# Kernel optimization log

Hardware: AMD Instinct MI355X
Metric: run time of the kernel (lower is better)

## Reference

```python
import jax, jax.numpy as jnp
import numpy as np

N, E, F_IN, H, G, C = 50000, 800000, 128, 4, 32, 4
NEG_SLOPE = 0.2
EPS_GN = 1e-5


def setup_inputs() -> dict:
    key = jax.random.key(0)
    ks = iter(jax.random.split(key, 64))
    def gl(shape, fan):
        return jax.random.normal(next(ks), shape, jnp.float32) / np.float32(np.sqrt(fan))
    inp = {}
    inp['x'] = jax.random.normal(next(ks), (N, F_IN), jnp.float32)
    inp['edge_index'] = jax.random.randint(next(ks), (2, E), 0, N, dtype=jnp.int32)
    inp['batch'] = jnp.sort(jax.random.randint(next(ks), (N,), 0, G, dtype=jnp.int32))
    inp['Wl1'] = gl((F_IN, H * 64), F_IN); inp['bl1'] = jnp.zeros((H * 64,), jnp.float32)
    inp['Wr1'] = gl((F_IN, H * 64), F_IN); inp['br1'] = jnp.zeros((H * 64,), jnp.float32)
    inp['att1'] = gl((H, 64), 64); inp['bias1'] = jnp.zeros((H * 64,), jnp.float32)
    inp['gw1'] = jnp.ones((H * 64,), jnp.float32); inp['gb1'] = jnp.zeros((H * 64,), jnp.float32); inp['ga1'] = jnp.ones((H * 64,), jnp.float32)
    inp['Wl2'] = gl((256, H * 32), 256); inp['bl2'] = jnp.zeros((H * 32,), jnp.float32)
    inp['Wr2'] = gl((256, H * 32), 256); inp['br2'] = jnp.zeros((H * 32,), jnp.float32)
    inp['att2'] = gl((H, 32), 32); inp['bias2'] = jnp.zeros((H * 32,), jnp.float32)
    inp['gw2'] = jnp.ones((H * 32,), jnp.float32); inp['gb2'] = jnp.zeros((H * 32,), jnp.float32); inp['ga2'] = jnp.ones((H * 32,), jnp.float32)
    # GATv2 layer 3: 128 -> 16, 4 heads averaged (concat=False)
    inp['Wl3'] = gl((128, H * 16), 128); inp['bl3'] = jnp.zeros((H * 16,), jnp.float32)
    inp['Wr3'] = gl((128, H * 16), 128); inp['br3'] = jnp.zeros((H * 16,), jnp.float32)
    inp['att3'] = gl((H, 16), 16); inp['bias3'] = jnp.zeros((16,), jnp.float32)
    inp['gw3'] = jnp.ones((16,), jnp.float32); inp['gb3'] = jnp.zeros((16,), jnp.float32); inp['ga3'] = jnp.ones((16,), jnp.float32)
    # final linear 16 -> C
    inp['linW'] = gl((16, C), 16); inp['linB'] = jnp.zeros((C,), jnp.float32)
    return inp


def _gatv2(x, src, dst, Wl, bl, Wr, br, att, bias, D, concat):
    n = x.shape[0]
    xl = (x @ Wl + bl).reshape(n, H, D)   # source-side transform
    xr = (x @ Wr + br).reshape(n, H, D)   # target-side transform
    m = xl[src] + xr[dst]                  # [E', H, D]
    s = jnp.einsum('ehd,hd->eh', jax.nn.leaky_relu(m, NEG_SLOPE), att)
    smax = jax.ops.segment_max(s, dst, num_segments=n)
    e = jnp.exp(s - smax[dst])
    denom = jax.ops.segment_sum(e, dst, num_segments=n)
    alpha = e / (denom[dst] + 1e-16)       # softmax over incoming edges
    out = jax.ops.segment_sum(alpha[:, :, None] * xl[src], dst, num_segments=n)
    out = out.reshape(n, H * D) if concat else out.mean(axis=1)
    return out + bias


def _graphnorm(x, batch, w, b, a):
    cnt = jnp.maximum(jax.ops.segment_sum(jnp.ones((x.shape[0],), x.dtype), batch, num_segments=G), 1.0)
    mean = jax.ops.segment_sum(x, batch, num_segments=G) / cnt[:, None]
    xc = x - a * mean[batch]
    var = jax.ops.segment_sum(xc * xc, batch, num_segments=G) / cnt[:, None]
    return w * xc / jnp.sqrt(var[batch] + EPS_GN) + b


def reference(x, edge_index, batch,
              Wl1, bl1, Wr1, br1, att1, bias1, gw1, gb1, ga1,
              Wl2, bl2, Wr2, br2, att2, bias2, gw2, gb2, ga2,
              Wl3, bl3, Wr3, br3, att3, bias3, gw3, gb3, ga3,
              linW, linB):
    n = x.shape[0]
    ar = jnp.arange(n, dtype=edge_index.dtype)
    src = jnp.concatenate([edge_index[0], ar])  # add self-loops (PyG default)
    dst = jnp.concatenate([edge_index[1], ar])
    h = jax.nn.relu(_graphnorm(_gatv2(x, src, dst, Wl1, bl1, Wr1, br1, att1, bias1, 64, True), batch, gw1, gb1, ga1))
    h = jax.nn.relu(_graphnorm(_gatv2(h, src, dst, Wl2, bl2, Wr2, br2, att2, bias2, 32, True), batch, gw2, gb2, ga2))
    h = jax.nn.relu(_graphnorm(_gatv2(h, src, dst, Wl3, bl3, Wr3, br3, att3, bias3, 16, False), batch, gw3, gb3, ga3))
    cnt = jnp.maximum(jax.ops.segment_sum(jnp.ones((n,), h.dtype), batch, num_segments=G), 1.0)
    features = jax.ops.segment_sum(h, batch, num_segments=G) / cnt[:, None]  # global mean pool [G,16]
    logits = features @ linW + linB
    return (logits, features)
```

## Files before the change

kernel.cpp:

```cpp
#include <hip/hip_runtime.h>
#include <cstdint>


#define NEG_SLOPE 0.2f

typedef __attribute__((ext_vector_type(8))) short short8;
typedef __attribute__((ext_vector_type(4))) float f32x4;
typedef _Float16 h2 __attribute__((ext_vector_type(2)));
union U16 { uint4 u; short8 s; };

__device__ inline unsigned short f2bf_rne(float x) {
  unsigned u = __float_as_uint(x);
  return (unsigned short)((u + 0x7fff + ((u >> 16) & 1)) >> 16);
}
__device__ inline unsigned short f2h_bits(float x) {
  _Float16 h = (_Float16)x;
  return __builtin_bit_cast(unsigned short, h);
}
__device__ inline float h2f(unsigned short h) {
  return (float)__builtin_bit_cast(_Float16, h);
}
__device__ inline h2 u2h2(unsigned u) { return __builtin_bit_cast(h2, u); }

__device__ inline float fdot2h(h2 a, h2 b, float c) {
#if __has_builtin(__builtin_amdgcn_fdot2)
  return __builtin_amdgcn_fdot2(a, b, c, false);
#else
  return c + (float)a.x * (float)b.x + (float)a.y * (float)b.y;
#endif
}

__device__ inline int wave_incl_scan(int v, int lane) {
#pragma unroll
  for (int ofs = 1; ofs < 64; ofs <<= 1) {
    int t = __shfl_up(v, ofs, 64);
    if (lane >= ofs) v += t;
  }
  return v;
}

__global__ void deg_batch_hist(const int* __restrict__ ei, const int* __restrict__ batch,
                               int* __restrict__ deg, int* __restrict__ cnt, int E, int N) {
  __shared__ int h[32];
  if (threadIdx.x < 32) h[threadIdx.x] = 0;
  __syncthreads();
  int i = blockIdx.x * blockDim.x + threadIdx.x;
  int ET = E + N;
  if (i < ET) {
    int d = (i < E) ? ei[E + i] : (i - E);
    atomicAdd(&deg[d], 1);
  }
  if (i < N) atomicAdd(&h[batch[i]], 1);
  __syncthreads();
  if (threadIdx.x < 32 && h[threadIdx.x] > 0) atomicAdd(&cnt[threadIdx.x], h[threadIdx.x]);
}

__global__ void chunk_sums(const int* __restrict__ deg, int* __restrict__ bsum, int n) {
  int tid = threadIdx.x, lane = tid & 63, wid = tid >> 6;
  int i = blockIdx.x * 1024 + tid;
  int v = (i < n) ? deg[i] : 0;
#pragma unroll
  for (int m = 32; m; m >>= 1) v += __shfl_xor(v, m, 64);
  __shared__ int ws[16];
  if (lane == 0) ws[wid] = v;
  __syncthreads();
  if (tid == 0) {
    int s = 0;
    for (int k = 0; k < 16; ++k) s += ws[k];
    bsum[blockIdx.x] = s;
  }
}

__global__ void scan_apply(const int* __restrict__ deg, const int* __restrict__ bsum,
                           int* __restrict__ off, int nb, int n) {
  __shared__ int ws[16];
  __shared__ int sb[64];
  int tid = threadIdx.x, lane = tid & 63, wid = tid >> 6;
  if (wid == 0) {
    int v = (lane < nb) ? bsum[lane] : 0;
    int incl = wave_incl_scan(v, lane);
    sb[lane] = incl;
  }
  __syncthreads();
  int boff = (blockIdx.x > 0) ? sb[blockIdx.x - 1] : 0;
  if (blockIdx.x == 0 && tid == 0) off[n] = sb[nb - 1];
  int i = blockIdx.x * 1024 + tid;
  int v = (i < n) ? deg[i] : 0;
  int incl = wave_incl_scan(v, lane);
  if (lane == 63) ws[wid] = incl;
  __syncthreads();
  if (wid == 0) {
    int t = (lane < 16) ? ws[lane] : 0;
    t = wave_incl_scan(t, lane);
    if (lane < 16) ws[lane] = t;
  }
  __syncthreads();
  int wpre = (wid > 0) ? ws[wid - 1] : 0;
  if (i < n) off[i] = boff + wpre + incl - v;
}

__global__ void scatter_edges(const int* __restrict__ ei, const int* __restrict__ off,
                              int* __restrict__ cur, int* __restrict__ csr_src,
                              int E, int N) {
  int i = blockIdx.x * blockDim.x + threadIdx.x;
  int ET = E + N;
  if (i >= ET) return;
  int s, d;
  if (i < E) { s = ei[i]; d = ei[E + i]; } else { s = d = i - E; }
  int pos = off[d] + atomicAdd(&cur[d], 1);
  csr_src[pos] = s;
}

__device__ inline void wprep_body(const float* __restrict__ W, unsigned short* __restrict__ pk,
                                  int K, int M, int t) {
  int nk = K >> 5;
  int total = (M >> 4) * nk * 512;
  if (t >= total) return;
  int j = t & 7;
  int l = (t >> 3) & 63;
  int rest = t >> 9;
  int kc = rest % nk;
  int ct = rest / nk;
  int k = (kc << 5) + ((l >> 4) << 3) + j;
  int col = (ct << 4) + (l & 15);
  float w = W[(size_t)k * M + col];
  unsigned u = __float_as_uint(w);
  unsigned short hi = (unsigned short)(u >> 16);
  float hif = __uint_as_float(u & 0xffff0000u);
  unsigned short lo = f2bf_rne(w - hif);
  unsigned short* dst = pk + ((size_t)(ct * nk + kc) * 64 + l) * 16;
  dst[j] = hi;
  dst[j + 8] = lo;
}

__global__ void wprep_all(const float* W0, const float* W1, const float* W2,
                          const float* W3, const float* W4, const float* W5,
                          unsigned short* p0, unsigned short* p1, unsigned short* p2,
                          unsigned short* p3, unsigned short* p4, unsigned short* p5) {
  int t = blockIdx.x * 256 + threadIdx.x;
  switch (blockIdx.y) {
    case 0: wprep_body(W0, p0, 128, 256, t); break;
    case 1: wprep_body(W1, p1, 128, 256, t); break;
    case 2: wprep_body(W2, p2, 256, 128, t); break;
    case 3: wprep_body(W3, p3, 256, 128, t); break;
    case 4: wprep_body(W4, p4, 128, 64, t); break;
    default: wprep_body(W5, p5, 128, 64, t); break;
  }
}

__device__ inline void gemm_epilogue(
    unsigned short* __restrict__ sb0, unsigned short* __restrict__ sb1,
    f32x4* accL, f32x4* accR,
    const float* __restrict__ biasL, const float* __restrict__ biasR,
    unsigned short* __restrict__ CL, unsigned short* __restrict__ CR,
    int N, int M, int c0g, int row0blk) {
  int wv = threadIdx.x >> 6, lane = threadIdx.x & 63;
  int lrow0 = wv * 16 + ((lane >> 4) << 2);
  int lcolb = lane & 15;
#pragma unroll
  for (int ct = 0; ct < 4; ++ct) {
    int lcol = (ct << 4) + lcolb;
    float bvL = biasL[(c0g << 4) + lcol];
    float bvR = biasR[(c0g << 4) + lcol];
#pragma unroll
    for (int r = 0; r < 4; ++r) {
      sb0[(lrow0 + r) * 72 + lcol] = f2h_bits(accL[ct][r] + bvL);
      sb1[(lrow0 + r) * 72 + lcol] = f2h_bits(accR[ct][r] + bvR);
    }
  }
  __syncthreads();
  int tid = threadIdx.x;
#pragma unroll
  for (int pass = 0; pass < 2; ++pass) {
    int row = (tid >> 3) + (pass << 5);
    int gr = row0blk + row;
    if (gr < N) {
      int co = (tid & 7) << 3;
      uint4 vL = *(const uint4*)&sb0[row * 72 + co];
      uint4 vR = *(const uint4*)&sb1[row * 72 + co];
      size_t go = (size_t)gr * M + (c0g << 4) + co;
      *(uint4*)(CL + go) = vL;
      *(uint4*)(CR + go) = vR;
    }
  }
}

__global__ __launch_bounds__(256) void gemm_f32a_dual(
    const float* __restrict__ A,
    const uint4* __restrict__ WpkL, const uint4* __restrict__ WpkR,
    const float* __restrict__ biasL, const float* __restrict__ biasR,
    unsigned short* __restrict__ CL, unsigned short* __restrict__ CR,
    int N, int K, int M) {
  __shared__ unsigned short sb[2][64 * 72];
  int wv = threadIdx.x >> 6, lane = threadIdx.x & 63;
  int r0 = blockIdx.y * 64 + wv * 16;
  int c0g = blockIdx.x << 2;
  int row = r0 + (lane & 15);
  int kq = (lane >> 4) << 3;
  int nk = K >> 5;
  bool rok = row < N;
  const float* arow = A + (size_t)row * K;
  f32x4 accL[4], accR[4];
#pragma unroll
  for (int i = 0; i < 4; ++i) { accL[i] = (f32x4){0,0,0,0}; accR[i] = (f32x4){0,0,0,0}; }
  for (int kc = 0; kc < nk; ++kc) {
    float av[8];
    if (rok) {
      float4 t0 = *(const float4*)(arow + (kc << 5) + kq);
      float4 t1 = *(const float4*)(arow + (kc << 5) + kq + 4);
      av[0] = t0.x; av[1] = t0.y; av[2] = t0.z; av[3] = t0.w;
      av[4] = t1.x; av[5] = t1.y; av[6] = t1.z; av[7] = t1.w;
    } else {
#pragma unroll
      for (int j = 0; j < 8; ++j) av[j] = 0.f;
    }
    short8 ahi, alo;
#pragma unroll
    for (int j = 0; j < 8; ++j) {
      unsigned u = __float_as_uint(av[j]);
      ahi[j] = (short)(u >> 16);
      float hif = __uint_as_float(u & 0xffff0000u);
      alo[j] = (short)f2bf_rne(av[j] - hif);
    }
#pragma unroll
    for (int ct = 0; ct < 4; ++ct) {
      size_t fo = (((size_t)(c0g + ct) * nk + kc) * 64 + lane) * 2;
      U16 bh, bl;
      bh.u = WpkL[fo]; bl.u = WpkL[fo + 1];
      accL[ct] = __builtin_amdgcn_mfma_f32_16x16x32_bf16(alo, bh.s, accL[ct], 0, 0, 0);
      accL[ct] = __builtin_amdgcn_mfma_f32_16x16x32_bf16(ahi, bl.s, accL[ct], 0, 0, 0);
      accL[ct] = __builtin_amdgcn_mfma_f32_16x16x32_bf16(ahi, bh.s, accL[ct], 0, 0, 0);
      bh.u = WpkR[fo]; bl.u = WpkR[fo + 1];
      accR[ct] = __builtin_amdgcn_mfma_f32_16x16x32_bf16(alo, bh.s, accR[ct], 0, 0, 0);
      accR[ct] = __builtin_amdgcn_mfma_f32_16x16x32_bf16(ahi, bl.s, accR[ct], 0, 0, 0);
      accR[ct] = __builtin_amdgcn_mfma_f32_16x16x32_bf16(ahi, bh.s, accR[ct], 0, 0, 0);
    }
  }
  gemm_epilogue(sb[0], sb[1], accL, accR, biasL, biasR, CL, CR, N, M, c0g, blockIdx.y * 64);
}

__global__ __launch_bounds__(256) void gemm_norm_dual(
    const unsigned short* __restrict__ A, const int* __restrict__ batch,
    const float* __restrict__ sc, const float* __restrict__ sh,
    const uint4* __restrict__ WpkL, const uint4* __restrict__ WpkR,
    const float* __restrict__ biasL, const float* __restrict__ biasR,
    unsigned short* __restrict__ CL, unsigned short* __restrict__ CR,
    int N, int K, int M) {
  __shared__ unsigned short sb[2][64 * 72];
  int wv = threadIdx.x >> 6, lane = threadIdx.x & 63;
  int r0 = blockIdx.y * 64 + wv * 16;
  int c0g = blockIdx.x << 2;
  int row = r0 + (lane & 15);
  int kq = (lane >> 4) << 3;
  int nk = K >> 5;
  bool rok = row < N;
  const unsigned short* arow = A + (size_t)row * K;
  int gF = rok ? batch[row] * K : 0;
  f32x4 accL[4], accR[4];
#pragma unroll
  for (int i = 0; i < 4; ++i) { accL[i] = (f32x4){0,0,0,0}; accR[i] = (f32x4){0,0,0,0}; }
  for (int kc = 0; kc < nk; ++kc) {
    short8 a;
    if (rok) {
      int kf = (kc << 5) + kq;
      uint4 araw = *(const uint4*)(arow + kf);
      float4 s0 = *(const float4*)(sc + gF + kf);
      float4 s1 = *(const float4*)(sc + gF + kf + 4);
      float4 h0 = *(const float4*)(sh + gF + kf);
      float4 h1 = *(const float4*)(sh + gF + kf + 4);
      h2 p0 = u2h2(araw.x), p1 = u2h2(araw.y), p2 = u2h2(araw.z), p3 = u2h2(araw.w);
      float y0 = fmaxf(fmaf((float)p0.x, s0.x, h0.x), 0.f);
      float y1 = fmaxf(fmaf((float)p0.y, s0.y, h0.y), 0.f);
      float y2 = fmaxf(fmaf((float)p1.x, s0.z, h0.z), 0.f);
      float y3 = fmaxf(fmaf((float)p1.y, s0.w, h0.w), 0.f);
      float y4 = fmaxf(fmaf((float)p2.x, s1.x, h1.x), 0.f);
      float y5 = fmaxf(fmaf((float)p2.y, s1.y, h1.y), 0.f);
      float y6 = fmaxf(fmaf((float)p3.x, s1.z, h1.z), 0.f);
      float y7 = fmaxf(fmaf((float)p3.y, s1.w, h1.w), 0.f);
      a[0] = (short)f2bf_rne(y0); a[1] = (short)f2bf_rne(y1);
      a[2] = (short)f2bf_rne(y2); a[3] = (short)f2bf_rne(y3);
      a[4] = (short)f2bf_rne(y4); a[5] = (short)f2bf_rne(y5);
      a[6] = (short)f2bf_rne(y6); a[7] = (short)f2bf_rne(y7);
    } else {
#pragma unroll
      for (int j = 0; j < 8; ++j) a[j] = 0;
    }
#pragma unroll
    for (int ct = 0; ct < 4; ++ct) {
      size_t fo = (((size_t)(c0g + ct) * nk + kc) * 64 + lane) * 2;
      U16 bh, bl;
      bh.u = WpkL[fo]; bl.u = WpkL[fo + 1];
      accL[ct] = __builtin_amdgcn_mfma_f32_16x16x32_bf16(a, bl.s, accL[ct], 0, 0, 0);
      accL[ct] = __builtin_amdgcn_mfma_f32_16x16x32_bf16(a, bh.s, accL[ct], 0, 0, 0);
      bh.u = WpkR[fo]; bl.u = WpkR[fo + 1];
      accR[ct] = __builtin_amdgcn_mfma_f32_16x16x32_bf16(a, bl.s, accR[ct], 0, 0, 0);
      accR[ct] = __builtin_amdgcn_mfma_f32_16x16x32_bf16(a, bh.s, accR[ct], 0, 0, 0);
    }
  }
  gemm_epilogue(sb[0], sb[1], accL, accR, biasL, biasR, CL, CR, N, M, c0g, blockIdx.y * 64);
}

template <int VEC> struct EO;

template <> struct EO<4> {
  using R = uint2;
  h2 xr0, xr1, at0, at1, sl;
  __device__ void init(const unsigned short* xrp, const float* ap) {
    uint2 rr = *(const uint2*)xrp;
    xr0 = u2h2(rr.x); xr1 = u2h2(rr.y);
    float4 a = *(const float4*)ap;
    at0 = (h2){(_Float16)a.x, (_Float16)a.y};
    at1 = (h2){(_Float16)a.z, (_Float16)a.w};
    sl = (h2){(_Float16)NEG_SLOPE, (_Float16)NEG_SLOPE};
  }
  static __device__ R ld(const unsigned short* base, unsigned off) {
    return *(const uint2*)(base + off);
  }
  __device__ float score(R r) const {
    h2 t0 = u2h2(r.x) + xr0;
    h2 t1 = u2h2(r.y) + xr1;
    t0 = __builtin_elementwise_max(t0, t0 * sl);
    t1 = __builtin_elementwise_max(t1, t1 * sl);
    return fdot2h(t0, at0, fdot2h(t1, at1, 0.f));
  }
  static __device__ void accum(R r, float p, float* o) {
    h2 x0 = u2h2(r.x), x1 = u2h2(r.y);
    o[0] = fmaf(p, (float)x0.x, o[0]);
    o[1] = fmaf(p, (float)x0.y, o[1]);
    o[2] = fmaf(p, (float)x1.x, o[2]);
    o[3] = fmaf(p, (float)x1.y, o[3]);
  }
};

template <> struct EO<2> {
  using R = unsigned;
  h2 xr0, at0, sl;
  __device__ void init(const unsigned short* xrp, const float* ap) {
    xr0 = u2h2(*(const unsigned*)xrp);
    float2 a = *(const float2*)ap;
    at0 = (h2){(_Float16)a.x, (_Float16)a.y};
    sl = (h2){(_Float16)NEG_SLOPE, (_Float16)NEG_SLOPE};
  }
  static __device__ R ld(const unsigned short* base, unsigned off) {
    return *(const unsigned*)(base + off);
  }
  __device__ float score(R r) const {
    h2 t0 = u2h2(r) + xr0;
    t0 = __builtin_elementwise_max(t0, t0 * sl);
    return fdot2h(t0, at0, 0.f);
  }
  static __device__ void accum(R r, float p, float* o) {
    h2 x0 = u2h2(r);
    o[0] = fmaf(p, (float)x0.x, o[0]);
    o[1] = fmaf(p, (float)x0.y, o[1]);
  }
};

template <> struct EO<1> {
  using R = unsigned short;
  float xrf, atf;
  __device__ void init(const unsigned short* xrp, const float* ap) {
    xrf = h2f(*xrp);
    atf = *ap;
  }
  static __device__ R ld(const unsigned short* base, unsigned off) {
    return base[off];
  }
  __device__ float score(R r) const {
    float t = h2f(r) + xrf;
    float lk = fmaxf(t, NEG_SLOPE * t);
    return lk * atf;
  }
  static __device__ void accum(R r, float p, float* o) {
    o[0] = fmaf(p, h2f(r), o[0]);
  }
};

template <int VEC, int C>
__device__ inline void gat_chunk(const unsigned short* __restrict__ xl,
                                 const int* __restrict__ csr_src, int j, int f0,
                                 const EO<VEC>& eo, float& lrun, float* o) {
  constexpr int HD = VEC * 64;
  typename EO<VEC>::R r[C];
#pragma unroll
  for (int c = 0; c < C; ++c)
    r[c] = EO<VEC>::ld(xl, (unsigned)csr_src[j + c] * HD + f0);
  float sc[C];
#pragma unroll
  for (int c = 0; c < C; ++c) sc[c] = eo.score(r[c]);
#pragma unroll
  for (int msk = 1; msk <= 8; msk <<= 1)
#pragma unroll
    for (int c = 0; c < C; ++c) sc[c] += __shfl_xor(sc[c], msk, 64);
  float p[C];
#pragma unroll
  for (int c = 0; c < C; ++c) p[c] = __expf(sc[c]);
#pragma unroll
  for (int c = 0; c < C; ++c) lrun += p[c];
#pragma unroll
  for (int c = 0; c < C; ++c) EO<VEC>::accum(r[c], p[c], o);
}

template <int VEC, bool MEANH, bool OUT16>
__global__ __launch_bounds__(256) void gat_fused(
    const unsigned short* __restrict__ xl, const unsigned short* __restrict__ xr,
    const float* __restrict__ att, const int* __restrict__ csr_src,
    const int* __restrict__ offp, const float* __restrict__ bias,
    void* __restrict__ outv, float* __restrict__ gsz, float* __restrict__ gqz,
    int n) {
  constexpr int HD = VEC * 64;
  {
    int zt = blockIdx.x * 256 + threadIdx.x;
    if (zt < 32 * 256) { gsz[zt] = 0.f; gqz[zt] = 0.f; }
  }
  int wave = (int)((blockIdx.x * (size_t)blockDim.x + threadIdx.x) >> 6);
  int lane = threadIdx.x & 63;
  if (wave >= n) return;
  const int f0 = lane * VEC;

  EO<VEC> eo;
  eo.init(xr + (size_t)wave * HD + f0, att + f0);

  float lrun = 0.f;
  float o[VEC];
#pragma unroll
  for (int v = 0; v < VEC; ++v) o[v] = 0.f;

  int beg = __builtin_amdgcn_readfirstlane(offp[wave]);
  int end = __builtin_amdgcn_readfirstlane(offp[wave + 1]);
  int j = beg;
  for (; j + 8 <= end; j += 8) gat_chunk<VEC, 8>(xl, csr_src, j, f0, eo, lrun, o);
  if (j + 4 <= end) { gat_chunk<VEC, 4>(xl, csr_src, j, f0, eo, lrun, o); j += 4; }
  for (; j < end; ++j) gat_chunk<VEC, 1>(xl, csr_src, j, f0, eo, lrun, o);

  float invl = 1.f / (lrun + 1e-16f);
  if (!MEANH) {
    if (OUT16) {
      unsigned short* out = (unsigned short*)outv;
#pragma unroll
      for (int v = 0; v < VEC; ++v)
        out[(size_t)wave * HD + f0 + v] = f2h_bits(o[v] * invl + bias[f0 + v]);
    } else {
      float* out = (float*)outv;
#pragma unroll
      for (int v = 0; v < VEC; ++v)
        out[(size_t)wave * HD + f0 + v] = o[v] * invl + bias[f0 + v];
    }
  } else {
    float val = o[0] * invl;
    val += __shfl_xor(val, 16, 64);
    val += __shfl_xor(val, 32, 64);
    val *= 0.25f;
    if (lane < 16) ((float*)outv)[(size_t)wave * 16 + lane] = val + bias[lane];
  }
}

template <int F>
__global__ void gn_stats_h(const unsigned short* __restrict__ x, const int* __restrict__ batch,
                           float* __restrict__ gsum, float* __restrict__ gsqs, int n) {
  constexpr int ROWS = 256 / F;
  int f = threadIdx.x % F;
  int r = threadIdx.x / F;
  int n0 = blockIdx.x * 128;
  float s = 0.f, q = 0.f;
  int curg = -1;
  for (int i = r; i < 128; i += ROWS) {
    int nn = n0 + i;
    if (nn >= n) break;
    int g = batch[nn];
    float v = h2f(x[(size_t)nn * F + f]);
    if (g != curg) {
      if (curg >= 0) { atomicAdd(&gsum[curg * F + f], s); atomicAdd(&gsqs[curg * F + f], q); }
      curg = g; s = 0.f; q = 0.f;
    }
    s += v; q += v * v;
  }
  if (curg >= 0) { atomicAdd(&gsum[curg * F + f], s); atomicAdd(&gsqs[curg * F + f], q); }
}

template <int F>
__global__ void gn_stats(const float* __restrict__ x, const int* __restrict__ batch,
                         float* __restrict__ gsum, float* __restrict__ gsqs, int n) {
  constexpr int ROWS = 256 / F;
  int f = threadIdx.x % F;
  int r = threadIdx.x / F;
  int n0 = blockIdx.x * 128;
  float s = 0.f, q = 0.f;
  int curg = -1;
  for (int i = r; i < 128; i += ROWS) {
    int nn = n0 + i;
    if (nn >= n) break;
    int g = batch[nn];
    float v = x[(size_t)nn * F + f];
    if (g != curg) {
      if (curg >= 0) { atomicAdd(&gsum[curg * F + f], s); atomicAdd(&gsqs[curg * F + f], q); }
      curg = g; s = 0.f; q = 0.f;
    }
    s += v; q += v * v;
  }
  if (curg >= 0) { atomicAdd(&gsum[curg * F + f], s); atomicAdd(&gsqs[curg * F + f], q); }
}

__global__ void gn_final(const float* __restrict__ gsum, const float* __restrict__ gsqs,
                         const int* __restrict__ cnt, const float* __restrict__ gw,
                         const float* __restrict__ gb, const float* __restrict__ ga,
                         float* __restrict__ sc, float* __restrict__ sh, int F) {
  int idx = blockIdx.x * blockDim.x + threadIdx.x;
  if (idx >= 32 * F) return;
  int g = idx / F, f = idx - g * F;
  float c = fmaxf((float)cnt[g], 1.f);
  float a = ga[f];
  float mu = gsum[idx] / c;
  float var = fmaxf(gsqs[idx] / c - (2.f * a - a * a) * mu * mu, 0.f);
  float rstd = rsqrtf(var + 1e-5f);
  float w = gw[f] * rstd;
  sc[idx] = w;
  sh[idx] = gb[f] - w * a * mu;
}

__global__ void norm_pool(const float* __restrict__ x, const int* __restrict__ batch,
                          const float* __restrict__ sc, const float* __restrict__ sh,
                          float* __restrict__ pooled, int n) {
  int f = threadIdx.x & 15;
  int r = threadIdx.x >> 4;
  int n0 = blockIdx.x * 128;
  float s = 0.f;
  int curg = -1;
  float scv = 0.f, shv = 0.f;
  for (int i = r; i < 128; i += 16) {
    int nn = n0 + i;
    if (nn >= n) break;
    int g = batch[nn];
    if (g != curg) {
      if (curg >= 0) atomicAdd(&pooled[curg * 16 + f], s);
      curg = g; s = 0.f;
      scv = sc[g * 16 + f];
      shv = sh[g * 16 + f];
    }
    float v = x[(size_t)nn * 16 + f];
    s += fmaxf(fmaf(v, scv, shv), 0.f);
  }
  if (curg >= 0) atomicAdd(&pooled[curg * 16 + f], s);
}

__global__ void finalize(const float* __restrict__ pooled, const int* __restrict__ cnt,
                         const float* __restrict__ linW, const float* __restrict__ linB,
                         float* __restrict__ out) {
  __shared__ float feat[32 * 16];
  int tid = threadIdx.x;
  {
    int g = tid >> 4;
    float c = fmaxf((float)cnt[g], 1.f);
    float v = pooled[tid] / c;
    feat[tid] = v;
    out[128 + tid] = v;
  }
  __syncthreads();
  if (tid < 128) {
    int g = tid >> 2, c = tid & 3;
    float s = linB[c];
#pragma unroll
    for (int k = 0; k < 16; ++k) s += feat[g * 16 + k] * linW[k * 4 + c];
    out[g * 4 + c] = s;
  }
}

extern "C" void kernel_launch(void* const* d_in, const int* in_sizes, int n_in,
                              void* d_out, int out_size, void* d_ws, size_t ws_size,
                              hipStream_t stream) {
  const float* x     = (const float*)d_in[0];
  const int*   ei    = (const int*)d_in[1];
  const int*   batch = (const int*)d_in[2];
  const float* Wl1 = (const float*)d_in[3];
  const float* bl1 = (const float*)d_in[4];
  const float* Wr1 = (const float*)d_in[5];
  const float* br1 = (const float*)d_in[6];
  const float* att1 = (const float*)d_in[7];
  const float* bias1 = (const float*)d_in[8];
  const float* gw1 = (const float*)d_in[9];
  const float* gb1 = (const float*)d_in[10];
  const float* ga1 = (const float*)d_in[11];
  const float* Wl2 = (const float*)d_in[12];
  const float* bl2 = (const float*)d_in[13];
  const float* Wr2 = (const float*)d_in[14];
  const float* br2 = (const float*)d_in[15];
  const float* att2 = (const float*)d_in[16];
  const float* bias2 = (const float*)d_in[17];
  const float* gw2 = (const float*)d_in[18];
  const float* gb2 = (const float*)d_in[19];
  const float* ga2 = (const float*)d_in[20];
  const float* Wl3 = (const float*)d_in[21];
  const float* bl3 = (const float*)d_in[22];
  const float* Wr3 = (const float*)d_in[23];
  const float* br3 = (const float*)d_in[24];
  const float* att3 = (const float*)d_in[25];
  const float* bias3 = (const float*)d_in[26];
  const float* gw3 = (const float*)d_in[27];
  const float* gb3 = (const float*)d_in[28];
  const float* ga3 = (const float*)d_in[29];
  const float* linW = (const float*)d_in[30];
  const float* linB = (const float*)d_in[31];
  float* out = (float*)d_out;

  const int N  = in_sizes[2];
  const int E  = in_sizes[1] / 2;
  const int ET = E + N;

  char* w = (char*)d_ws;
  float* P = (float*)w;             w += (size_t)N * 256 * 4;
  unsigned short* Ph = (unsigned short*)P;
  unsigned short* Qb = (unsigned short*)w; w += (size_t)N * 256 * 2;
  unsigned short* Rb = (unsigned short*)w; w += (size_t)N * 256 * 2;
  int* csr_src = (int*)w;           w += (size_t)ET * 4;
  int* offp = (int*)w;              w += (size_t)(N + 1) * 4;
  int* bsum = (int*)w;              w += 64 * 4;
  float* scb = (float*)w;           w += 32 * 256 * 4;
  float* shb = (float*)w;           w += 32 * 256 * 4;
  char* z0 = w;
  int* deg  = (int*)w;              w += (size_t)N * 4;
  int* cur  = (int*)w;              w += (size_t)N * 4;
  int* cnt  = (int*)w;              w += 32 * 4;
  float* pooled = (float*)w;        w += 512 * 4;
  float* gsum  = (float*)w;         w += 32 * 256 * 4;
  float* gsqs  = (float*)w;         w += 32 * 256 * 4;
  size_t zbytes = (size_t)(w - z0);
  uintptr_t wal = ((uintptr_t)w + 15) & ~(uintptr_t)15;
  uint4* wpk1l = (uint4*)wal;
  uint4* wpk1r = wpk1l + 8192;
  uint4* wpk2l = wpk1r + 8192;
  uint4* wpk2r = wpk2l + 8192;
  uint4* wpk3l = wpk2r + 8192;
  uint4* wpk3r = wpk3l + 2048;

  (void)hipMemsetAsync(z0, 0, zbytes, stream);

  wprep_all<<<dim3(128, 6), 256, 0, stream>>>(
      Wl1, Wr1, Wl2, Wr2, Wl3, Wr3,
      (unsigned short*)wpk1l, (unsigned short*)wpk1r,
      (unsigned short*)wpk2l, (unsigned short*)wpk2r,
      (unsigned short*)wpk3l, (unsigned short*)wpk3r);

  int nb = (N + 1023) / 1024;
  deg_batch_hist<<<(ET + 255) / 256, 256, 0, stream>>>(ei, batch, deg, cnt, E, N);
  chunk_sums<<<nb, 1024, 0, stream>>>(deg, bsum, N);
  scan_apply<<<nb, 1024, 0, stream>>>(deg, bsum, offp, nb, N);
  scatter_edges<<<(ET + 255) / 256, 256, 0, stream>>>(ei, offp, cur, csr_src, E, N);

  int gry = (N + 63) / 64;
  gemm_f32a_dual<<<dim3(4, gry), 256, 0, stream>>>(x, wpk1l, wpk1r, bl1, br1, Qb, Rb, N, 128, 256);
  gat_fused<4, false, true><<<(N + 3) / 4, 256, 0, stream>>>(Qb, Rb, att1, csr_src, offp, bias1, Ph, gsum, gsqs, N);
  gn_stats_h<256><<<(N + 127) / 128, 256, 0, stream>>>(Ph, batch, gsum, gsqs, N);
  gn_final<<<32, 256, 0, stream>>>(gsum, gsqs, cnt, gw1, gb1, ga1, scb, shb, 256);
  gemm_norm_dual<<<dim3(2, gry), 256, 0, stream>>>(Ph, batch, scb, shb, wpk2l, wpk2r, bl2, br2, Qb, Rb, N, 256, 128);
  gat_fused<2, false, true><<<(N + 3) / 4, 256, 0, stream>>>(Qb, Rb, att2, csr_src, offp, bias2, Ph, gsum, gsqs, N);
  gn_stats_h<128><<<(N + 127) / 128, 256, 0, stream>>>(Ph, batch, gsum, gsqs, N);
  gn_final<<<16, 256, 0, stream>>>(gsum, gsqs, cnt, gw2, gb2, ga2, scb, shb, 128);
  gemm_norm_dual<<<dim3(1, gry), 256, 0, stream>>>(Ph, batch, scb, shb, wpk3l, wpk3r, bl3, br3, Qb, Rb, N, 128, 64);
  gat_fused<1, true, false><<<(N + 3) / 4, 256, 0, stream>>>(Qb, Rb, att3, csr_src, offp, bias3, P, gsum, gsqs, N);
  gn_stats<16><<<(N + 127) / 128, 256, 0, stream>>>(P, batch, gsum, gsqs, N);
  gn_final<<<2, 256, 0, stream>>>(gsum, gsqs, cnt, gw3, gb3, ga3, scb, shb, 16);
  norm_pool<<<(N + 127) / 128, 256, 0, stream>>>(P, batch, scb, shb, pooled, N);
  finalize<<<1, 512, 0, stream>>>(pooled, cnt, linW, linB, out);
}
```

Before: 612.3 us.

## Fuse GraphNorm statistics into GAT aggregation and specialize GEMM dims

The per-layer GraphNorm sum and sum-of-squares reduction moves into the GAT aggregation kernel. Each block accumulates its outputs in shared memory when all its nodes belong to one graph, and falls back to global atomics otherwise. This removes three separate stats kernels and their re-read of the layer outputs. Zeroing of the stat buffers moves into gn_final after they are consumed. The GEMM kernels are templated on K and M so their k-loops can be unrolled, at the cost of more shared-atomic contention and extra syncs in the gather kernel.

```diff
diff --git a/kernel.cpp b/kernel.cpp
--- a/kernel.cpp
+++ b/kernel.cpp
@@ -185,24 +185,25 @@
   }
 }
 
+template <int K, int M>
 __global__ __launch_bounds__(256) void gemm_f32a_dual(
     const float* __restrict__ A,
     const uint4* __restrict__ WpkL, const uint4* __restrict__ WpkR,
     const float* __restrict__ biasL, const float* __restrict__ biasR,
-    unsigned short* __restrict__ CL, unsigned short* __restrict__ CR,
-    int N, int K, int M) {
+    unsigned short* __restrict__ CL, unsigned short* __restrict__ CR, int N) {
+  constexpr int nk = K >> 5;
   __shared__ unsigned short sb[2][64 * 72];
   int wv = threadIdx.x >> 6, lane = threadIdx.x & 63;
   int r0 = blockIdx.y * 64 + wv * 16;
   int c0g = blockIdx.x << 2;
   int row = r0 + (lane & 15);
   int kq = (lane >> 4) << 3;
-  int nk = K >> 5;
   bool rok = row < N;
   const float* arow = A + (size_t)row * K;
   f32x4 accL[4], accR[4];
 #pragma unroll
   for (int i = 0; i < 4; ++i) { accL[i] = (f32x4){0,0,0,0}; accR[i] = (f32x4){0,0,0,0}; }
+#pragma unroll
   for (int kc = 0; kc < nk; ++kc) {
     float av[8];
     if (rok) {
@@ -239,26 +240,27 @@
   gemm_epilogue(sb[0], sb[1], accL, accR, biasL, biasR, CL, CR, N, M, c0g, blockIdx.y * 64);
 }
 
+template <int K, int M>
 __global__ __launch_bounds__(256) void gemm_norm_dual(
     const unsigned short* __restrict__ A, const int* __restrict__ batch,
     const float* __restrict__ sc, const float* __restrict__ sh,
     const uint4* __restrict__ WpkL, const uint4* __restrict__ WpkR,
     const float* __restrict__ biasL, const float* __restrict__ biasR,
-    unsigned short* __restrict__ CL, unsigned short* __restrict__ CR,
-    int N, int K, int M) {
+    unsigned short* __restrict__ CL, unsigned short* __restrict__ CR, int N) {
+  constexpr int nk = K >> 5;
   __shared__ unsigned short sb[2][64 * 72];
   int wv = threadIdx.x >> 6, lane = threadIdx.x & 63;
   int r0 = blockIdx.y * 64 + wv * 16;
   int c0g = blockIdx.x << 2;
   int row = r0 + (lane & 15);
   int kq = (lane >> 4) << 3;
-  int nk = K >> 5;
   bool rok = row < N;
   const unsigned short* arow = A + (size_t)row * K;
   int gF = rok ? batch[row] * K : 0;
   f32x4 accL[4], accR[4];
 #pragma unroll
   for (int i = 0; i < 4; ++i) { accL[i] = (f32x4){0,0,0,0}; accR[i] = (f32x4){0,0,0,0}; }
+#pragma unroll 2
   for (int kc = 0; kc < nk; ++kc) {
     short8 a;
     if (rok) {
@@ -405,103 +407,99 @@
 __global__ __launch_bounds__(256) void gat_fused(
     const unsigned short* __restrict__ xl, const unsigned short* __restrict__ xr,
     const float* __restrict__ att, const int* __restrict__ csr_src,
-    const int* __restrict__ offp, const float* __restrict__ bias,
-    void* __restrict__ outv, float* __restrict__ gsz, float* __restrict__ gqz,
-    int n) {
+    const int* __restrict__ offp, const int* __restrict__ batch,
+    const float* __restrict__ bias, void* __restrict__ outv,
+    float* __restrict__ gsum, float* __restrict__ gsqs, int n) {
   constexpr int HD = VEC * 64;
-  {
-    int zt = blockIdx.x * 256 + threadIdx.x;
-    if (zt < 32 * 256) { gsz[zt] = 0.f; gqz[zt] = 0.f; }
-  }
-  int wave = (int)((blockIdx.x * (size_t)blockDim.x + threadIdx.x) >> 6);
+  constexpr int F = MEANH ? 16 : HD;
+  __shared__ float ssum[F];
+  __shared__ float ssq[F];
+  if (threadIdx.x < F) { ssum[threadIdx.x] = 0.f; ssq[threadIdx.x] = 0.f; }
+  int wave = blockIdx.x * 4 + (threadIdx.x >> 6);
   int lane = threadIdx.x & 63;
-  if (wave >= n) return;
+  bool active = wave < n;
+  int nb0 = blockIdx.x * 4; if (nb0 >= n) nb0 = n - 1;
+  int nb3 = blockIdx.x * 4 + 3; if (nb3 >= n) nb3 = n - 1;
+  int g0 = batch[nb0];
+  bool uni = (batch[nb3] == g0);
+  __syncthreads();
+
   const int f0 = lane * VEC;
-
-  EO<VEC> eo;
-  eo.init(xr + (size_t)wave * HD + f0, att + f0);
-
+  float o[VEC];
   float lrun = 0.f;
-  float o[VEC];
+  int g = g0;
 #pragma unroll
   for (int v = 0; v < VEC; ++v) o[v] = 0.f;
-
-  int beg = __builtin_amdgcn_readfirstlane(offp[wave]);
-  int end = __builtin_amdgcn_readfirstlane(offp[wave + 1]);
-  int j = beg;
-  for (; j + 8 <= end; j += 8) gat_chunk<VEC, 8>(xl, csr_src, j, f0, eo, lrun, o);
-  if (j + 4 <= end) { gat_chunk<VEC, 4>(xl, csr_src, j, f0, eo, lrun, o); j += 4; }
-  for (; j < end; ++j) gat_chunk<VEC, 1>(xl, csr_src, j, f0, eo, lrun, o);
-
+  if (active) {
+    EO<VEC> eo;
+    eo.init(xr + (size_t)wave * HD + f0, att + f0);
+    int beg = __builtin_amdgcn_readfirstlane(offp[wave]);
+    int end = __builtin_amdgcn_readfirstlane(offp[wave + 1]);
+    int j = beg;
+    for (; j + 8 <= end; j += 8) gat_chunk<VEC, 8>(xl, csr_src, j, f0, eo, lrun, o);
+    if (j + 4 <= end) { gat_chunk<VEC, 4>(xl, csr_src, j, f0, eo, lrun, o); j += 4; }
+    for (; j < end; ++j) gat_chunk<VEC, 1>(xl, csr_src, j, f0, eo, lrun, o);
+    g = batch[wave];
+  }
   float invl = 1.f / (lrun + 1e-16f);
+
   if (!MEANH) {
-    if (OUT16) {
-      unsigned short* out = (unsigned short*)outv;
-#pragma unroll
-      for (int v = 0; v < VEC; ++v)
-        out[(size_t)wave * HD + f0 + v] = f2h_bits(o[v] * invl + bias[f0 + v]);
-    } else {
-      float* out = (float*)outv;
-#pragma unroll
-      for (int v = 0; v < VEC; ++v)
-        out[(size_t)wave * HD + f0 + v] = o[v] * invl + bias[f0 + v];
+    if (active) {
+      unsigned short* out16 = (unsigned short*)outv;
+      float* out32 = (float*)outv;
+#pragma unroll
+      for (int v = 0; v < VEC; ++v) {
+        float y = o[v] * invl + bias[f0 + v];
+        float yr;
+        if (OUT16) {
+          unsigned short hb = f2h_bits(y);
+          out16[(size_t)wave * HD + f0 + v] = hb;
+          yr = h2f(hb);
+        } else {
+          out32[(size_t)wave * HD + f0 + v] = y;
+          yr = y;
+        }
+        if (uni) {
+          atomicAdd(&ssum[f0 + v], yr);
+          atomicAdd(&ssq[f0 + v], yr * yr);
+        } else {
+          atomicAdd(&gsum[g * F + f0 + v], yr);
+          atomicAdd(&gsqs[g * F + f0 + v], yr * yr);
+        }
+      }
+    }
+    __syncthreads();
+    if (uni && threadIdx.x < F) {
+      atomicAdd(&gsum[g0 * F + threadIdx.x], ssum[threadIdx.x]);
+      atomicAdd(&gsqs[g0 * F + threadIdx.x], ssq[threadIdx.x]);
     }
   } else {
-    float val = o[0] * invl;
-    val += __shfl_xor(val, 16, 64);
-    val += __shfl_xor(val, 32, 64);
-    val *= 0.25f;
-    if (lane < 16) ((float*)outv)[(size_t)wave * 16 + lane] = val + bias[lane];
-  }
-}
-
-template <int F>
-__global__ void gn_stats_h(const unsigned short* __restrict__ x, const int* __restrict__ batch,
-                           float* __restrict__ gsum, float* __restrict__ gsqs, int n) {
-  constexpr int ROWS = 256 / F;
-  int f = threadIdx.x % F;
-  int r = threadIdx.x / F;
-  int n0 = blockIdx.x * 128;
-  float s = 0.f, q = 0.f;
-  int curg = -1;
-  for (int i = r; i < 128; i += ROWS) {
-    int nn = n0 + i;
-    if (nn >= n) break;
-    int g = batch[nn];
-    float v = h2f(x[(size_t)nn * F + f]);
-    if (g != curg) {
-      if (curg >= 0) { atomicAdd(&gsum[curg * F + f], s); atomicAdd(&gsqs[curg * F + f], q); }
-      curg = g; s = 0.f; q = 0.f;
-    }
-    s += v; q += v * v;
-  }
-  if (curg >= 0) { atomicAdd(&gsum[curg * F + f], s); atomicAdd(&gsqs[curg * F + f], q); }
-}
-
-template <int F>
-__global__ void gn_stats(const float* __restrict__ x, const int* __restrict__ batch,
-                         float* __restrict__ gsum, float* __restrict__ gsqs, int n) {
-  constexpr int ROWS = 256 / F;
-  int f = threadIdx.x % F;
-  int r = threadIdx.x / F;
-  int n0 = blockIdx.x * 128;
-  float s = 0.f, q = 0.f;
-  int curg = -1;
-  for (int i = r; i < 128; i += ROWS) {
-    int nn = n0 + i;
-    if (nn >= n) break;
-    int g = batch[nn];
-    float v = x[(size_t)nn * F + f];
-    if (g != curg) {
-      if (curg >= 0) { atomicAdd(&gsum[curg * F + f], s); atomicAdd(&gsqs[curg * F + f], q); }
-      curg = g; s = 0.f; q = 0.f;
-    }
-    s += v; q += v * v;
-  }
-  if (curg >= 0) { atomicAdd(&gsum[curg * F + f], s); atomicAdd(&gsqs[curg * F + f], q); }
-}
-
-__global__ void gn_final(const float* __restrict__ gsum, const float* __restrict__ gsqs,
+    if (active) {
+      float val = o[0] * invl;
+      val += __shfl_xor(val, 16, 64);
+      val += __shfl_xor(val, 32, 64);
+      val *= 0.25f;
+      if (lane < 16) {
+        float y = val + bias[lane];
+        ((float*)outv)[(size_t)wave * 16 + lane] = y;
+        if (uni) {
+          atomicAdd(&ssum[lane], y);
+          atomicAdd(&ssq[lane], y * y);
+        } else {
+          atomicAdd(&gsum[g * 16 + lane], y);
+          atomicAdd(&gsqs[g * 16 + lane], y * y);
+        }
+      }
+    }
+    __syncthreads();
+    if (uni && threadIdx.x < 16) {
+      atomicAdd(&gsum[g0 * 16 + threadIdx.x], ssum[threadIdx.x]);
+      atomicAdd(&gsqs[g0 * 16 + threadIdx.x], ssq[threadIdx.x]);
+    }
+  }
+}
+
+__global__ void gn_final(float* __restrict__ gsum, float* __restrict__ gsqs,
                          const int* __restrict__ cnt, const float* __restrict__ gw,
                          const float* __restrict__ gb, const float* __restrict__ ga,
                          float* __restrict__ sc, float* __restrict__ sh, int F) {
@@ -516,6 +514,8 @@
   float w = gw[f] * rstd;
   sc[idx] = w;
   sh[idx] = gb[f] - w * a * mu;
+  gsum[idx] = 0.f;
+  gsqs[idx] = 0.f;
 }
 
 __global__ void norm_pool(const float* __restrict__ x, const int* __restrict__ batch,
@@ -647,17 +647,14 @@
   scatter_edges<<<(ET + 255) / 256, 256, 0, stream>>>(ei, offp, cur, csr_src, E, N);
 
   int gry = (N + 63) / 64;
-  gemm_f32a_dual<<<dim3(4, gry), 256, 0, stream>>>(x, wpk1l, wpk1r, bl1, br1, Qb, Rb, N, 128, 256);
-  gat_fused<4, false, true><<<(N + 3) / 4, 256, 0, stream>>>(Qb, Rb, att1, csr_src, offp, bias1, Ph, gsum, gsqs, N);
-  gn_stats_h<256><<<(N + 127) / 128, 256, 0, stream>>>(Ph, batch, gsum, gsqs, N);
+  gemm_f32a_dual<128, 256><<<dim3(4, gry), 256, 0, stream>>>(x, wpk1l, wpk1r, bl1, br1, Qb, Rb, N);
+  gat_fused<4, false, true><<<(N + 3) / 4, 256, 0, stream>>>(Qb, Rb, att1, csr_src, offp, batch, bias1, Ph, gsum, gsqs, N);
   gn_final<<<32, 256, 0, stream>>>(gsum, gsqs, cnt, gw1, gb1, ga1, scb, shb, 256);
-  gemm_norm_dual<<<dim3(2, gry), 256, 0, stream>>>(Ph, batch, scb, shb, wpk2l, wpk2r, bl2, br2, Qb, Rb, N, 256, 128);
-  gat_fused<2, false, true><<<(N + 3) / 4, 256, 0, stream>>>(Qb, Rb, att2, csr_src, offp, bias2, Ph, gsum, gsqs, N);
-  gn_stats_h<128><<<(N + 127) / 128, 256, 0, stream>>>(Ph, batch, gsum, gsqs, N);
+  gemm_norm_dual<256, 128><<<dim3(2, gry), 256, 0, stream>>>(Ph, batch, scb, shb, wpk2l, wpk2r, bl2, br2, Qb, Rb, N);
+  gat_fused<2, false, true><<<(N + 3) / 4, 256, 0, stream>>>(Qb, Rb, att2, csr_src, offp, batch, bias2, Ph, gsum, gsqs, N);
   gn_final<<<16, 256, 0, stream>>>(gsum, gsqs, cnt, gw2, gb2, ga2, scb, shb, 128);
-  gemm_norm_dual<<<dim3(1, gry), 256, 0, stream>>>(Ph, batch, scb, shb, wpk3l, wpk3r, bl3, br3, Qb, Rb, N, 128, 64);
-  gat_fused<1, true, false><<<(N + 3) / 4, 256, 0, stream>>>(Qb, Rb, att3, csr_src, offp, bias3, P, gsum, gsqs, N);
-  gn_stats<16><<<(N + 127) / 128, 256, 0, stream>>>(P, batch, gsum, gsqs, N);
+  gemm_norm_dual<128, 64><<<dim3(1, gry), 256, 0, stream>>>(Ph, batch, scb, shb, wpk3l, wpk3r, bl3, br3, Qb, Rb, N);
+  gat_fused<1, true, false><<<(N + 3) / 4, 256, 0, stream>>>(Qb, Rb, att3, csr_src, offp, batch, bias3, P, gsum, gsqs, N);
   gn_final<<<2, 256, 0, stream>>>(gsum, gsqs, cnt, gw3, gb3, ga3, scb, shb, 16);
   norm_pool<<<(N + 127) / 128, 256, 0, stream>>>(P, batch, scb, shb, pooled, N);
   finalize<<<1, 512, 0, stream>>>(pooled, cnt, linW, linB, out);
```

After: 783.6 us. 1.28x slower.
